# Optimization experiments

Measured on AMD Instinct MI355X. Metric: run time of the kernel, lower is better.

The kernel has to match this reference:

```python
import jax, jax.numpy as jnp
import numpy as np

L, D, H, N, B2 = 9, 256, 4, 1024, 4   # layers, embed dim, heads, keypoints, 2*pairs
HD = D // H
THR = 0.1
MAXM = 50


def _linear(x, W, b):
    return x @ W.T + b


def _ln(x, g, b, eps=1e-5):
    m = jnp.mean(x, -1, keepdims=True)
    v = jnp.var(x, -1, keepdims=True)
    return (x - m) * jax.lax.rsqrt(v + eps) * g + b


def _ffn(x, w1, b1, g, bb, w2, b2):
    h = _linear(x, w1, b1)
    h = jax.nn.gelu(_ln(h, g, bb), approximate=False)
    return _linear(h, w2, b2)


def _mha(q, k, v):
    b, nq, _ = q.shape
    nk = k.shape[1]
    qh = q.reshape(b, nq, H, HD)
    kh = k.reshape(b, nk, H, HD)
    vh = v.reshape(b, nk, H, HD)
    s = jnp.einsum('bqhd,bkhd->bhqk', qh, kh) * (1.0 / np.float32(np.sqrt(HD)))
    a = jax.nn.softmax(s, -1)
    return jnp.einsum('bhqk,bkhd->bqhd', a, vh).reshape(b, nq, D)


def _rotate_half(qk):  # qk: [b, n, D, 2]
    b, n, _, _ = qk.shape
    r = qk.reshape(b, n, H, HD // 2, 2, 2)
    r = jnp.stack([-r[..., 1, :], r[..., 0, :]], axis=4)
    return r.reshape(b, n, D, 2)


def _posenc(kpts, Wr):
    proj = kpts @ Wr.T                    # [b, n, HD//2]
    def expand(t):
        t = jnp.repeat(t, 2, axis=-1)     # interleave -> [b, n, HD]
        return jnp.tile(t, (1, 1, H))     # -> [b, n, D]
    return jnp.stack([expand(jnp.cos(proj)), expand(jnp.sin(proj))])  # [2, b, n, D]


def _forward(kpts, desc, posenc_Wr,
             sWqkv_w, sWqkv_b, sOut_w, sOut_b, sF1_w, sF1_b, sLN_g, sLN_b, sF2_w, sF2_b,
             cQK_w, cQK_b, cV_w, cV_b, cOut_w, cOut_b, cF1_w, cF1_b, cLN_g, cLN_b, cF2_w, cF2_b,
             fp_w, fp_b, match_w, match_b):
    enc = _posenc(kpts, posenc_Wr)
    x = desc
    idx = np.arange(B2)
    swap = idx // 2 * 2 + (1 - idx % 2)   # swap images within each pair
    for i in range(L):
        # ---- self attention with cached rotary encoding ----
        b, n, _ = x.shape
        qkv = _linear(x, sWqkv_w[i], sWqkv_b[i]).reshape(b, n, D, 3)
        qk, v = qkv[..., :2], qkv[..., 2]
        qk = enc[0][..., None] * qk + enc[1][..., None] * _rotate_half(qk)
        ctx = _mha(qk[..., 0], qk[..., 1], v)
        msg = _linear(ctx, sOut_w[i], sOut_b[i])
        x = x + _ffn(jnp.concatenate([x, msg], -1),
                     sF1_w[i], sF1_b[i], sLN_g[i], sLN_b[i], sF2_w[i], sF2_b[i])
        # ---- cross attention between images of each pair ----
        qk = _linear(x, cQK_w[i], cQK_b[i])
        v = _linear(x, cV_w[i], cV_b[i])
        m = _mha(qk, qk[swap], v[swap])
        m = _linear(m, cOut_w[i], cOut_b[i])
        x = x + _ffn(jnp.concatenate([x, m], -1),
                     cF1_w[i], cF1_b[i], cLN_g[i], cLN_b[i], cF2_w[i], cF2_b[i])
    # ---- match assignment: sigmoid log double softmax ----
    md = _linear(x, fp_w, fp_b) / (D ** 0.25)
    sim = jnp.einsum('bnd,bmd->bnm', md[0::2], md[1::2])
    z = _linear(x, match_w, match_b)      # [B2, N, 1]
    cert = jax.nn.log_sigmoid(z[0::2]) + jnp.swapaxes(jax.nn.log_sigmoid(z[1::2]), 1, 2)
    return jax.nn.log_softmax(sim, 2) + jax.nn.log_softmax(sim, 1) + cert


def _filter_matches(scores):
    B = scores.shape[0]
    m0 = jnp.argmax(scores, 2)
    m1 = jnp.argmax(scores, 1)
    mscores = jnp.exp(jnp.max(scores, 2))
    mutual = jnp.arange(N)[None, :] == jnp.take_along_axis(m1, m0, 1)
    masked = mscores * ((mscores > THR) & mutual).astype(mscores.dtype)
    topk_scores, topk_idx = jax.lax.top_k(masked, MAXM)
    topk_m1 = jnp.take_along_axis(m0, topk_idx, 1)
    b_idx = jnp.broadcast_to(jnp.arange(B)[:, None], (B, MAXM))
    matches = jnp.stack([b_idx, topk_idx, topk_m1], 2)
    return matches[0], topk_scores[0]


def setup_inputs() -> dict:
    key = jax.random.key(0)
    ks = iter(jax.random.split(key, 48))
    def w(shape, scale=0.02):
        return jax.random.normal(next(ks), shape, jnp.float32) * scale
    inp = {
        'kpts': jax.random.normal(next(ks), (B2, N, 2), jnp.float32),
        'desc': jax.random.normal(next(ks), (B2, N, D), jnp.float32),
        'posenc_Wr': w((HD // 2, 2), 1.0),  # std = gamma**-2 = 1
        'sWqkv_w': w((L, 3 * D, D)), 'sWqkv_b': w((L, 3 * D)),
        'sOut_w': w((L, D, D)), 'sOut_b': w((L, D)),
        'sF1_w': w((L, 2 * D, 2 * D)), 'sF1_b': w((L, 2 * D)),
        'sLN_g': jnp.ones((L, 2 * D), jnp.float32), 'sLN_b': jnp.zeros((L, 2 * D), jnp.float32),
        'sF2_w': w((L, D, 2 * D)), 'sF2_b': w((L, D)),
        'cQK_w': w((L, D, D)), 'cQK_b': w((L, D)),
        'cV_w': w((L, D, D)), 'cV_b': w((L, D)),
        'cOut_w': w((L, D, D)), 'cOut_b': w((L, D)),
        'cF1_w': w((L, 2 * D, 2 * D)), 'cF1_b': w((L, 2 * D)),
        'cLN_g': jnp.ones((L, 2 * D), jnp.float32), 'cLN_b': jnp.zeros((L, 2 * D), jnp.float32),
        'cF2_w': w((L, D, 2 * D)), 'cF2_b': w((L, D)),
        'fp_w': w((D, D)), 'fp_b': w((D,)),
        'match_w': w((1, D)), 'match_b': w((1,)),
    }
    return inp


def reference(kpts, desc, posenc_Wr,
              sWqkv_w, sWqkv_b, sOut_w, sOut_b, sF1_w, sF1_b, sLN_g, sLN_b, sF2_w, sF2_b,
              cQK_w, cQK_b, cV_w, cV_b, cOut_w, cOut_b, cF1_w, cF1_b, cLN_g, cLN_b, cF2_w, cF2_b,
              fp_w, fp_b, match_w, match_b):
    scores = _forward(kpts, desc, posenc_Wr,
                      sWqkv_w, sWqkv_b, sOut_w, sOut_b, sF1_w, sF1_b, sLN_g, sLN_b, sF2_w, sF2_b,
                      cQK_w, cQK_b, cV_w, cV_b, cOut_w, cOut_b, cF1_w, cF1_b, cLN_g, cLN_b, cF2_w, cF2_b,
                      fp_w, fp_b, match_w, match_b)
    matches, mscores = _filter_matches(scores)
    return scores, matches, mscores
```

## Files before the change

### kernel.cpp

```cpp
#include <hip/hip_runtime.h>
#include <hip/hip_bf16.h>
#include <math.h>

typedef __hip_bfloat16 bf16;
typedef unsigned short ushort;
typedef unsigned int u32;
typedef __attribute__((ext_vector_type(8))) short s8b;
typedef __attribute__((ext_vector_type(4))) short s4b;
typedef __attribute__((ext_vector_type(4))) float f4v;

#define Nc 1024
#define Dc 256
#define MA 4096

__device__ __forceinline__ float tofl(float v){ return v; }
__device__ __forceinline__ float tofl(bf16 v){ return __bfloat162float(v); }

__device__ __forceinline__ ushort rneu(float f){
  unsigned u = __float_as_uint(f);
  unsigned r = (u + 0x7fffu + ((u>>16)&1u)) >> 16;
  return (ushort)r;
}
__device__ __forceinline__ float ubf(ushort h){ return __uint_as_float(((unsigned)h)<<16); }

__device__ __forceinline__ float fexp2(float x){
#if __has_builtin(__builtin_amdgcn_exp2f)
  return __builtin_amdgcn_exp2f(x);
#else
  return exp2f(x);
#endif
}

__global__ void k_detect(const void* p, int* flag){
  if(threadIdx.x==0 && blockIdx.x==0){
    *flag = (((const ushort*)p)[0] == 0x3F80) ? 0 : 1;
  }
}

template<typename TIN>
__device__ void gemm_body(const float* A, const TIN* B, const TIN* bias, float* C,
                          int M, int Nout, int K, int lda, int ldb, int ldc,
                          float alpha, int accum, int dolog){
  __shared__ float As[32][33];
  __shared__ float Bs[32][33];
  int tx = threadIdx.x, ty = threadIdx.y;
  int tid = ty*16 + tx;
  int n0 = blockIdx.x*32, m0 = blockIdx.y*32;
  int lr = tid >> 3;
  int lc = (tid & 7) * 4;
  float acc00=0.f, acc01=0.f, acc10=0.f, acc11=0.f;
  for(int kk=0; kk<K; kk+=32){
    int m = m0 + lr, n = n0 + lr;
#pragma unroll
    for(int j=0;j<4;j++){
      int k = kk + lc + j;
      As[lr][lc+j] = (m < M && k < K) ? A[(size_t)m*lda + k] : 0.f;
      Bs[lr][lc+j] = (n < Nout && k < K) ? tofl(B[(size_t)n*ldb + k]) : 0.f;
    }
    __syncthreads();
#pragma unroll
    for(int k=0;k<32;k++){
      float a0 = As[ty][k],   a1 = As[ty+16][k];
      float b0 = Bs[tx][k],   b1 = Bs[tx+16][k];
      acc00 += a0*b0; acc01 += a0*b1; acc10 += a1*b0; acc11 += a1*b1;
    }
    __syncthreads();
  }
#define STORE(mm,nn,acc) do{ int m_=(mm), n_=(nn); if(m_<M && n_<Nout){ \
    float r = (acc) + (bias ? tofl(bias[n_]) : 0.f); r *= alpha; \
    if(dolog) r = fminf(r,0.f) - log1pf(expf(-fabsf(r))); \
    if(accum) C[(size_t)m_*ldc + n_] += r; else C[(size_t)m_*ldc + n_] = r; } }while(0)
  STORE(m0+ty,    n0+tx,    acc00);
  STORE(m0+ty,    n0+tx+16, acc01);
  STORE(m0+ty+16, n0+tx,    acc10);
  STORE(m0+ty+16, n0+tx+16, acc11);
#undef STORE
}

__global__ __launch_bounds__(256)
void k_gemm_w(const int* flag, const float* A, const void* Bb, long boff,
              const void* biasb, long biasoff, float* C,
              int M, int Nout, int K, int lda, int ldb, int ldc,
              float alpha, int accum, int dolog){
  if(*flag){
    const float* B = ((const float*)Bb) + boff;
    const float* bi = biasb ? ((const float*)biasb) + biasoff : nullptr;
    gemm_body<float>(A, B, bi, C, M, Nout, K, lda, ldb, ldc, alpha, accum, dolog);
  }else{
    const bf16* B = ((const bf16*)Bb) + boff;
    const bf16* bi = biasb ? ((const bf16*)biasb) + biasoff : nullptr;
    gemm_body<bf16>(A, B, bi, C, M, Nout, K, lda, ldb, ldc, alpha, accum, dolog);
  }
}

template<typename TIN>
__device__ void cast2_body(const void* in_, float* x, ushort* xh, ushort* xl, int n){
  const TIN* in = (const TIN*)in_;
  int i = blockIdx.x*256 + threadIdx.x;
  if(i >= n) return;
  float f = tofl(in[i]);
  x[i] = f;
  ushort h = rneu(f);
  xh[i] = h; xl[i] = rneu(f - ubf(h));
}
__global__ void k_cast2(const int* flag, const void* in, float* x, ushort* xh, ushort* xl, int n){
  if(*flag) cast2_body<float>(in, x, xh, xl, n); else cast2_body<bf16>(in, x, xh, xl, n);
}

template<typename TIN>
__device__ void splitw_body(const void* src_, long off, ushort* dh, ushort* dl, int n){
  const TIN* src = ((const TIN*)src_) + off;
  int i = blockIdx.x*256 + threadIdx.x;
  if(i >= n) return;
  float f = tofl(src[i]);
  ushort h = rneu(f);
  dh[i] = h; dl[i] = rneu(f - ubf(h));
}
__global__ void k_splitw(const int* flag, const void* src, long off, ushort* dh, ushort* dl, int n){
  if(*flag) splitw_body<float>(src, off, dh, dl, n); else splitw_body<bf16>(src, off, dh, dl, n);
}
template<typename TIN>
__device__ void biasf_body(const void* src_, long off, float* dst, int n){
  const TIN* src = ((const TIN*)src_) + off;
  int i = blockIdx.x*256 + threadIdx.x;
  if(i < n) dst[i] = tofl(src[i]);
}
__global__ void k_biasf(const int* flag, const void* src, long off, float* dst, int n){
  if(*flag) biasf_body<float>(src, off, dst, n); else biasf_body<bf16>(src, off, dst, n);
}

template<typename TIN>
__device__ void rotcs_body(const void* kpts_, const void* Wr_, float* cs){
  int i = blockIdx.x*256 + threadIdx.x;
  if(i >= MA*32) return;
  int m = i >> 5, p = i & 31;
  const TIN* kpts = (const TIN*)kpts_;
  const TIN* Wr   = (const TIN*)Wr_;
  float kx = tofl(kpts[m*2]), ky = tofl(kpts[m*2+1]);
  float proj = kx*tofl(Wr[p*2]) + ky*tofl(Wr[p*2+1]);
  cs[(size_t)m*64 + p*2    ] = cosf(proj);
  cs[(size_t)m*64 + p*2 + 1] = sinf(proj);
}
__global__ void k_rotcs(const int* flag, const void* kpts, const void* Wr, float* cs){
  if(*flag) rotcs_body<float>(kpts, Wr, cs); else rotcs_body<bf16>(kpts, Wr, cs);
}

template<typename TIN>
__device__ void wsl_body(int L, const void* p0,const void* p1,const void* p2,const void* p3,
                         const void* p4,const void* p5,const void* p6,const void* p7,const void* p8,
                         const void* b0,const void* b1,const void* b2,const void* b3,const void* b4,
                         const void* b5,const void* b6,const void* b7,const void* b8,
                         ushort* WH, ushort* WL, float* WB){
  int idx = blockIdx.x*256 + threadIdx.x;
  if(idx < 311296){
    int i = idx*4;
    const TIN* s = nullptr;
    const TIN* tb = nullptr; int trow = 0, tcol = 0;
    if(i < 196608){
      int nr = i >> 8, col = i & 255;
      int sr = (nr < 256) ? nr*3 : (nr < 512) ? (nr-256)*3+1 : (nr-512)*3+2;
      s = (const TIN*)p0 + (size_t)L*196608 + sr*256 + col;
    }
    else if(i < 262144){ int li = i-196608; tb = (const TIN*)p1 + (size_t)L*65536; trow = li>>8; tcol = li&255; }
    else if(i < 524288)  s = (const TIN*)p2 + (size_t)L*262144 + (i-262144);
    else if(i < 655360)  s = (const TIN*)p3 + (size_t)L*131072 + (i-524288);
    else if(i < 720896)  s = (const TIN*)p4 + (size_t)L*65536  + (i-655360);
    else if(i < 786432)  s = (const TIN*)p5 + (size_t)L*65536  + (i-720896);
    else if(i < 851968){ int li = i-786432; tb = (const TIN*)p6 + (size_t)L*65536; trow = li>>8; tcol = li&255; }
    else if(i < 1114112) s = (const TIN*)p7 + (size_t)L*262144 + (i-851968);
    else                 s = (const TIN*)p8 + (size_t)L*131072 + (i-1114112);
    float f[4];
    if(tb){
#pragma unroll
      for(int j=0;j<4;j++) f[j] = tofl(tb[(size_t)(tcol+j)*256 + trow]);
    } else if constexpr(sizeof(TIN) == 4){
      f4v v = *(const f4v*)s;
      f[0]=v[0]; f[1]=v[1]; f[2]=v[2]; f[3]=v[3];
    } else {
      s4b v = *(const s4b*)s;
#pragma unroll
      for(int j=0;j<4;j++) f[j] = __uint_as_float(((u32)(ushort)v[j])<<16);
    }
    s4b hv, lv;
#pragma unroll
    for(int j=0;j<4;j++){
      ushort h = rneu(f[j]);
      hv[j] = (short)h;
      lv[j] = (short)rneu(f[j] - ubf(h));
    }
    *(s4b*)&WH[i] = hv;
    *(s4b*)&WL[i] = lv;
  } else if(idx < 311296 + 3328){
    int j = idx - 311296;
    const TIN* s;
    if(j < 768){
      int sj = (j < 256) ? j*3 : (j < 512) ? (j-256)*3+1 : (j-512)*3+2;
      s = (const TIN*)b0 + (size_t)L*768 + sj;
    }
    else if(j < 1024)  s = (const TIN*)b1 + (size_t)L*256 + (j-768);
    else if(j < 1536)  s = (const TIN*)b2 + (size_t)L*512 + (j-1024);
    else if(j < 1792)  s = (const TIN*)b3 + (size_t)L*256 + (j-1536);
    else if(j < 2048)  s = (const TIN*)b4 + (size_t)L*256 + (j-1792);
    else if(j < 2304)  s = (const TIN*)b5 + (size_t)L*256 + (j-2048);
    else if(j < 2560)  s = (const TIN*)b6 + (size_t)L*256 + (j-2304);
    else if(j < 3072)  s = (const TIN*)b7 + (size_t)L*512 + (j-2560);
    else               s = (const TIN*)b8 + (size_t)L*256 + (j-3072);
    WB[j] = tofl(*s);
  }
}
__global__ void k_wsplit(const int* flag, int L0, long strW, long strB,
    const void* p0,const void* p1,const void* p2,const void* p3,const void* p4,
    const void* p5,const void* p6,const void* p7,const void* p8,
    const void* b0,const void* b1,const void* b2,const void* b3,const void* b4,
    const void* b5,const void* b6,const void* b7,const void* b8,
    ushort* WH, ushort* WL, float* WB){
  int L = L0 + blockIdx.y;
  ushort* WHl = WH + (size_t)blockIdx.y*strW;
  ushort* WLl = WL + (size_t)blockIdx.y*strW;
  float*  WBl = WB + (size_t)blockIdx.y*strB;
  if(*flag) wsl_body<float>(L,p0,p1,p2,p3,p4,p5,p6,p7,p8,b0,b1,b2,b3,b4,b5,b6,b7,b8,WHl,WLl,WBl);
  else      wsl_body<bf16>(L,p0,p1,p2,p3,p4,p5,p6,p7,p8,b0,b1,b2,b3,b4,b5,b6,b7,b8,WHl,WLl,WBl);
}

__global__ __launch_bounds__(256)
void k_bcomb(const ushort* __restrict__ WH, const ushort* __restrict__ WL,
             float* WB, long strW, long strB){
  __shared__ float bo[256];
  int bx = blockIdx.x;
  int c = blockIdx.y;
  int L = c >> 1, br = c & 1;
  size_t wbase = (size_t)L*strW + (br ? 851968 : 262144);
  float* WBl = WB + (size_t)L*strB;
  float* b1 = WBl + (br ? 2560 : 1024);
  const float* bout = WBl + (br ? 2304 : 768);
  int t = threadIdx.x;
  bo[t] = bout[t];
  __syncthreads();
  int o = bx*64 + (t>>2);
  int p = t & 3;
  size_t rb = wbase + (size_t)o*512 + 256;
  float s = 0.f;
  for(int j=p*64; j<p*64+64; j++){
    s += (ubf(WH[rb+j]) + ubf(WL[rb+j])) * bo[j];
  }
  s += __shfl_xor(s,1);
  s += __shfl_xor(s,2);
  if(p==0) b1[o] += s;
}

template<int MT>
__global__ __launch_bounds__(256)
void k_gemm_mxT(const ushort* __restrict__ Ah, const ushort* __restrict__ Al,
                const ushort* __restrict__ A2h, const ushort* __restrict__ A2l, int lda,
                const ushort* __restrict__ Bh, const ushort* __restrict__ Bl, int ldb,
                const float* __restrict__ bias, float alpha,
                float* C, int ldc, int accum,
                ushort* Ch, ushort* Cl, int lds,
                ushort* keh, ushort* kel, const float* __restrict__ cs,
                ushort* vth, ushort* vtl,
                int K, int mode){
  constexpr int MFR = MT/16;
  constexpr int NACC = MFR*2;
  constexpr int MFH = MFR/2;
  __shared__ __align__(16) ushort LB[(2*MT+128)*72];
  int t = threadIdx.x;
  int n0 = blockIdx.x*64, m0 = blockIdx.y*MT;
  size_t wofs4 = 0;
  if(mode == 4){
    int by = blockIdx.y;
    int combo = by >> 4;
    m0 = (by & 15) * MT;
    int Lc = combo >> 1, br = combo & 1;
    size_t basec = (size_t)Lc * (size_t)lds;
    wofs4 = basec + (br ? 851968 : 262144) + 256;
    size_t oofs = basec + (br ? 786432 : 196608);
    Bh = Ah + oofs; Bl = Al + oofs; ldb = 256;
    Ah = Ah + wofs4; Al = Al + wofs4; lda = 512;
  }
  int w = t>>6, lane = t&63, quad = lane>>4, l15 = lane&15;
  int kg = w>>1, nh = w&1;
  int brow = t>>2, bc16 = (t&3)*16;
  int arow = (MT==64) ? (t>>2) : (t>>3);
  int acol = (MT==64) ? ((t&3)*16) : ((t&7)*8);
  f4v acc[NACC];
  f4v zz = {0.f,0.f,0.f,0.f};
#pragma unroll
  for(int j=0;j<NACC;j++) acc[j] = zz;
  int rounds = K >> 6;

  s8b r0,r1,r2,r3,r4,r5,r6,r7;
  auto gload = [&](int r){
    int k0 = r*64;
    const ushort* ah = Ah; const ushort* al = Al; int kloc = k0;
    if(A2h && k0 >= 256){ ah = A2h; al = A2l; kloc = k0 - 256; }
    const ushort* aph = &ah[(size_t)(m0+arow)*lda + kloc + acol];
    const ushort* apl = &al[(size_t)(m0+arow)*lda + kloc + acol];
    const ushort* bph = &Bh[(size_t)(n0+brow)*ldb + k0 + bc16];
    const ushort* bpl = &Bl[(size_t)(n0+brow)*ldb + k0 + bc16];
    r0 = *(const s8b*)aph;
    r2 = *(const s8b*)apl;
    if(MT==64){ r1 = *(const s8b*)(aph+8); r3 = *(const s8b*)(apl+8); }
    r4 = *(const s8b*)bph;   r5 = *(const s8b*)(bph+8);
    r6 = *(const s8b*)bpl;   r7 = *(const s8b*)(bpl+8);
  };
  auto writeS = [&](){
    *(s8b*)&LB[(arow)*72 + acol]        = r0;
    *(s8b*)&LB[(MT+arow)*72 + acol]     = r2;
    if(MT==64){
      *(s8b*)&LB[(arow)*72 + acol+8]    = r1;
      *(s8b*)&LB[(MT+arow)*72 + acol+8] = r3;
    }
    *(s8b*)&LB[(2*MT+brow)*72 + bc16]      = r4;
    *(s8b*)&LB[(2*MT+brow)*72 + bc16+8]    = r5;
    *(s8b*)&LB[(2*MT+64+brow)*72 + bc16]   = r6;
    *(s8b*)&LB[(2*MT+64+brow)*72 + bc16+8] = r7;
  };

  gload(0);
  for(int r=0; r<rounds; r++){
    __syncthreads();
    writeS();
    __syncthreads();
    s8b afh[MFR], afl[MFR], bfh[2], bfl[2];
#pragma unroll
    for(int mf=0;mf<MFR;mf++){
      afh[mf] = *(s8b*)&LB[(mf*16+l15)*72 + kg*32+quad*8];
      afl[mf] = *(s8b*)&LB[(MT+mf*16+l15)*72 + kg*32+quad*8];
    }
#pragma unroll
    for(int nf=0;nf<2;nf++){
      bfh[nf] = *(s8b*)&LB[(2*MT+nh*32+nf*16+l15)*72 + kg*32+quad*8];
      bfl[nf] = *(s8b*)&LB[(2*MT+64+nh*32+nf*16+l15)*72 + kg*32+quad*8];
    }
    if(r+1 < rounds) gload(r+1);
#pragma unroll
    for(int mf=0;mf<MFR;mf++){
#pragma unroll
      for(int nf=0;nf<2;nf++){
        int a = mf*2+nf;
        acc[a] = __builtin_amdgcn_mfma_f32_16x16x32_bf16(afh[mf], bfh[nf], acc[a], 0,0,0);
        acc[a] = __builtin_amdgcn_mfma_f32_16x16x32_bf16(afh[mf], bfl[nf], acc[a], 0,0,0);
        acc[a] = __builtin_amdgcn_mfma_f32_16x16x32_bf16(afl[mf], bfh[nf], acc[a], 0,0,0);
      }
    }
  }
  __syncthreads();
  f4v* scr = (f4v*)LB;
#pragma unroll
  for(int f=0;f<NACC;f++) scr[(w*NACC+f)*64 + lane] = acc[f];
  __syncthreads();
  int pw = w^2;
#pragma unroll
  for(int f=0;f<NACC;f++){
    f4v o = scr[(pw*NACC+f)*64 + lane];
    acc[f] += o;
  }

  bool vblk = (mode == 1 && n0 >= 512) || (mode == 3 && n0 >= 256);
  if(vblk){
    __syncthreads();
    u32* tp = (u32*)LB;
#pragma unroll
    for(int mi=0;mi<MFH;mi++){
      int mf = kg*MFH + mi;
#pragma unroll
      for(int nf=0;nf<2;nf++){
        f4v a = acc[mf*2+nf];
#pragma unroll
        for(int rr=0;rr<4;rr++){
          int ml = mf*16 + quad*4 + rr;
          int nl = nh*32 + nf*16 + l15;
          float val = a[rr];
          if(bias) val += bias[n0 + nl];
          val *= alpha;
          ushort hh = rneu(val);
          ushort ll = rneu(val - ubf(hh));
          tp[nl*(MT+1) + ml] = (u32)hh | ((u32)ll << 16);
        }
      }
    }
    __syncthreads();
    int b = m0 >> 10;
    int mloc = m0 & 1023;
    int d0 = n0 - ((mode == 1) ? 512 : 256);
    constexpr int NPASS = (MT==64) ? 2 : 1;
#pragma unroll
    for(int pass=0; pass<NPASS; pass++){
      int row, col;
      if(MT==64){ row = (t>>3) + pass*32; col = (t&7)*8; }
      else      { row = t>>2;             col = (t&3)*8; }
      int d = d0 + row;
      u32 c0=tp[row*(MT+1)+col+0], c1=tp[row*(MT+1)+col+1], c2=tp[row*(MT+1)+col+2], c3=tp[row*(MT+1)+col+3];
      u32 c4=tp[row*(MT+1)+col+4], c5=tp[row*(MT+1)+col+5], c6=tp[row*(MT+1)+col+6], c7=tp[row*(MT+1)+col+7];
      s8b hi, lo;
      hi[0]=(short)(c0&0xffff); lo[0]=(short)(c0>>16);
      hi[1]=(short)(c1&0xffff); lo[1]=(short)(c1>>16);
      hi[2]=(short)(c2&0xffff); lo[2]=(short)(c2>>16);
      hi[3]=(short)(c3&0xffff); lo[3]=(short)(c3>>16);
      hi[4]=(short)(c4&0xffff); lo[4]=(short)(c4>>16);
      hi[5]=(short)(c5&0xffff); lo[5]=(short)(c5>>16);
      hi[6]=(short)(c6&0xffff); lo[6]=(short)(c6>>16);
      hi[7]=(short)(c7&0xffff); lo[7]=(short)(c7>>16);
      size_t go = ((size_t)((b*4 + (d>>6))*64 + (d&63)))*1024 + mloc + col;
      *(s8b*)&vth[go] = hi;
      *(s8b*)&vtl[go] = lo;
    }
    return;
  }

#pragma unroll
  for(int mi=0;mi<MFH;mi++){
    int mf = kg*MFH + mi;
#pragma unroll
    for(int nf=0;nf<2;nf++){
      f4v a = acc[mf*2+nf];
#pragma unroll
      for(int rr=0;rr<4;rr++){
        int m = m0 + mf*16 + quad*4 + rr;
        int n = n0 + nh*32 + nf*16 + l15;
        float val = a[rr];
        if(bias) val += bias[n];
        val *= alpha;
        if(mode == 1){
          int d = (n < 256) ? n : (n - 256);
          const float* csp = cs + (size_t)m*64 + (d & 62);
          float cc = csp[0], ssn = csp[1];
          float pv = __shfl_xor(val, 1);
          float rv = (d & 1) ? (cc*val + ssn*pv) : (cc*val - ssn*pv);
          ushort hh = rneu(rv);
          ushort* dh = (n < 256) ? Ch : keh;
          ushort* dl = (n < 256) ? Cl : kel;
          size_t gi = (size_t)m*256 + d;
          dh[gi] = hh; dl[gi] = rneu(rv - ubf(hh));
        } else if(mode == 3){
          ushort hh = rneu(val);
          Ch[(size_t)m*256 + n] = hh;
          Cl[(size_t)m*256 + n] = rneu(val - ubf(hh));
        } else if(mode == 4){
          ushort hh = rneu(val);
          size_t gi = wofs4 + (size_t)m*512 + n;
          Ch[gi] = hh;
          Cl[gi] = rneu(val - ubf(hh));
        } else {
          if(C){
            size_t ci = (size_t)m*ldc + n;
            if(accum) val += C[ci];
            C[ci] = val;
          }
          if(Ch){
            ushort hh = rneu(val);
            Ch[(size_t)m*lds + n] = hh;
            Cl[(size_t)m*lds + n] = rneu(val - ubf(hh));
          }
        }
      }
    }
  }
}

#define FSC 0.18033688011112042f
__global__ __launch_bounds__(256)
void k_flashmx(const ushort* __restrict__ qh_, const ushort* __restrict__ ql_,
               const ushort* __restrict__ kh_, const ushort* __restrict__ kl_,
               const ushort* __restrict__ vth_, const ushort* __restrict__ vtl_,
               ushort* __restrict__ cth, ushort* __restrict__ ctl, int bxor,
               float* __restrict__ PO, float* __restrict__ PML, int nch){
  int qt = blockIdx.x, z = blockIdx.y, ch = blockIdx.z;
  int b = z>>2, h = z&3;
  int bk = b ^ bxor;
  __shared__ __align__(16) ushort Kh[64][72], Kl[64][72], Vh[64][72], Vl[64][72];
  int t = threadIdx.x, w = t>>6, lane = t&63, quad = lane>>4, l15 = lane&15;
  ushort* Psw = &Kh[w*16][0];
  s8b qfh[2], qfl[2];
  {
    size_t row = (size_t)b*1024 + qt*64 + w*16 + l15;
    const ushort* qrh = qh_ + row*256 + h*64;
    const ushort* qrl = ql_ + row*256 + h*64;
    qfh[0] = *(const s8b*)(qrh + quad*8);
    qfh[1] = *(const s8b*)(qrh + 32 + quad*8);
    qfl[0] = *(const s8b*)(qrl + quad*8);
    qfl[1] = *(const s8b*)(qrl + 32 + quad*8);
  }
  float m_i[4] = {-1e30f,-1e30f,-1e30f,-1e30f};
  float l_i[4] = {0.f,0.f,0.f,0.f};
  f4v O[4];
  f4v zz = {0.f,0.f,0.f,0.f};
#pragma unroll
  for(int dt=0;dt<4;dt++) O[dt] = zz;

  s8b rK0,rK1,rK2,rK3, rV0,rV1,rV2,rV3;
  auto stage_load = [&](int kt){
#pragma unroll
    for(int i=0;i<4;i++){
      int c = t + i*256;
      int half = c>>9, row = (c>>3)&63, o8 = (c&7)*8;
      const s8b* src = (const s8b*)((half ? kl_ : kh_) +
                       ((size_t)(bk*1024 + kt*64 + row))*256 + h*64 + o8);
      if(i==0) rK0=*src; else if(i==1) rK1=*src; else if(i==2) rK2=*src; else rK3=*src;
    }
#pragma unroll
    for(int i=0;i<4;i++){
      int c = t + i*256;
      int half = c>>9, d = (c>>3)&63, o8 = (c&7)*8;
      const s8b* src = (const s8b*)((half ? vtl_ : vth_) +
                       ((size_t)((bk*4+h)*64 + d))*1024 + kt*64 + o8);
      if(i==0) rV0=*src; else if(i==1) rV1=*src; else if(i==2) rV2=*src; else rV3=*src;
    }
  };
  auto stage_write = [&](){
#pragma unroll
    for(int i=0;i<4;i++){
      int c = t + i*256;
      int half = c>>9, row = (c>>3)&63, o8 = (c&7)*8;
      s8b v = (i==0)?rK0:(i==1)?rK1:(i==2)?rK2:rK3;
      if(half) *(s8b*)&Kl[row][o8] = v;
      else     *(s8b*)&Kh[row][o8] = v;
    }
#pragma unroll
    for(int i=0;i<4;i++){
      int c = t + i*256;
      int half = c>>9, d = (c>>3)&63, o8 = (c&7)*8;
      s8b v = (i==0)?rV0:(i==1)?rV1:(i==2)?rV2:rV3;
      if(half) *(s8b*)&Vl[d][o8] = v;
      else     *(s8b*)&Vh[d][o8] = v;
    }
  };

  int ktn = 16/nch;
  int kt0 = ch*ktn;
  stage_load(kt0);
  for(int kt=kt0; kt<kt0+ktn; kt++){
    __syncthreads();
    stage_write();
    __syncthreads();
    if(kt+1 < kt0+ktn) stage_load(kt+1);
    f4v s[4];
#pragma unroll
    for(int nt=0;nt<4;nt++) s[nt] = zz;
#pragma unroll
    for(int nt=0;nt<4;nt++){
#pragma unroll
      for(int k2=0;k2<2;k2++){
        s8b fbh = *(s8b*)&Kh[nt*16+l15][k2*32 + quad*8];
        s8b fbl = *(s8b*)&Kl[nt*16+l15][k2*32 + quad*8];
        s[nt] = __builtin_amdgcn_mfma_f32_16x16x32_bf16(qfh[k2], fbh, s[nt], 0,0,0);
        s[nt] = __builtin_amdgcn_mfma_f32_16x16x32_bf16(qfh[k2], fbl, s[nt], 0,0,0);
        s[nt] = __builtin_amdgcn_mfma_f32_16x16x32_bf16(qfl[k2], fbh, s[nt], 0,0,0);
      }
    }
    __syncthreads();
#pragma unroll
    for(int rr=0;rr<4;rr++){
      float v0=s[0][rr]*FSC, v1=s[1][rr]*FSC, v2=s[2][rr]*FSC, v3=s[3][rr]*FSC;
      float mx = fmaxf(fmaxf(v0,v1), fmaxf(v2,v3));
      mx = fmaxf(mx, __shfl_xor(mx,1));
      mx = fmaxf(mx, __shfl_xor(mx,2));
      mx = fmaxf(mx, __shfl_xor(mx,4));
      mx = fmaxf(mx, __shfl_xor(mx,8));
      float mnew = fmaxf(m_i[rr], mx);
      float al = fexp2(m_i[rr] - mnew);
      float p0 = fexp2(v0-mnew), p1 = fexp2(v1-mnew), p2 = fexp2(v2-mnew), p3 = fexp2(v3-mnew);
      float ls = p0+p1+p2+p3;
      ls += __shfl_xor(ls,1);
      ls += __shfl_xor(ls,2);
      ls += __shfl_xor(ls,4);
      ls += __shfl_xor(ls,8);
      l_i[rr] = l_i[rr]*al + ls;
      m_i[rr] = mnew;
#pragma unroll
      for(int dt=0;dt<4;dt++) O[dt][rr] *= al;
      int prow = quad*4 + rr;
      Psw[prow*72 +  0 + l15] = rneu(p0);
      Psw[prow*72 + 16 + l15] = rneu(p1);
      Psw[prow*72 + 32 + l15] = rneu(p2);
      Psw[prow*72 + 48 + l15] = rneu(p3);
    }
    s8b pf0 = *(s8b*)&Psw[l15*72 + quad*8];
    s8b pf1 = *(s8b*)&Psw[l15*72 + 32 + quad*8];
#pragma unroll
    for(int dt=0;dt<4;dt++){
#pragma unroll
      for(int k2=0;k2<2;k2++){
        s8b fvh = *(s8b*)&Vh[dt*16+l15][k2*32 + quad*8];
        s8b fvl = *(s8b*)&Vl[dt*16+l15][k2*32 + quad*8];
        s8b pf = k2 ? pf1 : pf0;
        O[dt] = __builtin_amdgcn_mfma_f32_16x16x32_bf16(pf, fvh, O[dt], 0,0,0);
        O[dt] = __builtin_amdgcn_mfma_f32_16x16x32_bf16(pf, fvl, O[dt], 0,0,0);
      }
    }
  }
  if(nch == 1){
#pragma unroll
    for(int rr=0;rr<4;rr++){
      float inv = 1.f / l_i[rr];
      int row = qt*64 + w*16 + quad*4 + rr;
#pragma unroll
      for(int dt=0;dt<4;dt++){
        float val = O[dt][rr]*inv;
        size_t gi = ((size_t)b*1024 + row)*256 + h*64 + dt*16 + l15;
        ushort hh = rneu(val);
        cth[gi] = hh; ctl[gi] = rneu(val - ubf(hh));
      }
    }
  } else {
    size_t tb = (size_t)(z*16+qt)*nch + ch;
    float* po  = PO  + tb*4096;
    float* pml = PML + tb*128;
#pragma unroll
    for(int rr=0;rr<4;rr++){
      int row = w*16 + quad*4 + rr;
#pragma unroll
      for(int dt=0;dt<4;dt++){
        po[row*64 + dt*16 + l15] = O[dt][rr];
      }
      if(l15 == 0){
        pml[row]      = m_i[rr];
        pml[64 + row] = l_i[rr];
      }
    }
  }
}

__global__ __launch_bounds__(256)
void k_fmerge(const float* __restrict__ PO, const float* __restrict__ PML,
              ushort* __restrict__ cth, ushort* __restrict__ ctl){
  int qt = blockIdx.x, z = blockIdx.y;
  int b = z>>2, h = z&3;
  int t = threadIdx.x;
  int row = t>>2, dg = (t&3)*16;
  size_t tb0 = (size_t)(z*16+qt)*4;
  float m0 = PML[(tb0+0)*128 + row], m1 = PML[(tb0+1)*128 + row];
  float m2 = PML[(tb0+2)*128 + row], m3 = PML[(tb0+3)*128 + row];
  float M = fmaxf(fmaxf(m0,m1), fmaxf(m2,m3));
  float w0 = fexp2(m0-M), w1 = fexp2(m1-M), w2 = fexp2(m2-M), w3 = fexp2(m3-M);
  float L = PML[(tb0+0)*128 + 64 + row]*w0 + PML[(tb0+1)*128 + 64 + row]*w1
          + PML[(tb0+2)*128 + 64 + row]*w2 + PML[(tb0+3)*128 + 64 + row]*w3;
  float inv = 1.f/L;
  const f4v* p0 = (const f4v*)(PO + (tb0+0)*4096 + row*64 + dg);
  const f4v* p1 = (const f4v*)(PO + (tb0+1)*4096 + row*64 + dg);
  const f4v* p2 = (const f4v*)(PO + (tb0+2)*4096 + row*64 + dg);
  const f4v* p3 = (const f4v*)(PO + (tb0+3)*4096 + row*64 + dg);
  size_t gi = ((size_t)b*1024 + qt*64 + row)*256 + h*64 + dg;
#pragma unroll
  for(int j=0;j<4;j++){
    f4v o = p0[j]*w0 + p1[j]*w1 + p2[j]*w2 + p3[j]*w3;
#pragma unroll
    for(int e=0;e<4;e++){
      float val = o[e]*inv;
      ushort hh = rneu(val);
      cth[gi + j*4 + e] = hh;
      ctl[gi + j*4 + e] = rneu(val - ubf(hh));
    }
  }
}

template<typename TIN>
__device__ void ln2_body(const float* h, ushort* hh, ushort* hl, const TIN* g, const TIN* bb){
  __shared__ float ws8[8];
  int r = blockIdx.x; int t = threadIdx.x;
  int w = t>>6, lane = t&63;
  const float* row = h + (size_t)r*512;
  float a = row[t], b_ = row[t+256];
  float s = a + b_;
#pragma unroll
  for(int off=1; off<64; off<<=1) s += __shfl_xor(s, off);
  if(lane==0) ws8[w] = s;
  __syncthreads();
  float mean = (ws8[0]+ws8[1]+ws8[2]+ws8[3])*(1.f/512.f);
  float da = a-mean, db = b_-mean;
  float v = da*da + db*db;
#pragma unroll
  for(int off=1; off<64; off<<=1) v += __shfl_xor(v, off);
  if(lane==0) ws8[4+w] = v;
  __syncthreads();
  float rstd = rsqrtf((ws8[4]+ws8[5]+ws8[6]+ws8[7])*(1.f/512.f) + 1e-5f);
  float na = da*rstd*tofl(g[t])     + tofl(bb[t]);
  float nb = db*rstd*tofl(g[t+256]) + tofl(bb[t+256]);
  float ga = 0.5f*na*(1.f + erff(na*0.70710678f));
  float gb = 0.5f*nb*(1.f + erff(nb*0.70710678f));
  size_t base = (size_t)r*512;
  ushort u0 = rneu(ga); hh[base+t] = u0; hl[base+t] = rneu(ga - ubf(u0));
  ushort u1 = rneu(gb); hh[base+t+256] = u1; hl[base+t+256] = rneu(gb - ubf(u1));
}
__global__ void k_ln_gelu2(const int* flag, const float* h, ushort* hh, ushort* hl,
                           const void* gb, long goff, const void* bbb, long boff){
  if(*flag) ln2_body<float>(h, hh, hl, ((const float*)gb)+goff, ((const float*)bbb)+boff);
  else      ln2_body<bf16>(h, hh, hl, ((const bf16*)gb)+goff, ((const bf16*)bbb)+boff);
}

__global__ void k_lse_cols2(const float* __restrict__ simbase, float* __restrict__ clseb){
  __shared__ float Rm[16][16], Rs[16][16];
  int blk = blockIdx.x;
  int p = blk >> 6, bx = blk & 63;
  const float* sim = simbase + (size_t)p*1048576;
  float* clse = clseb + p*1024;
  int t = threadIdx.x;
  int c = t & 15, s = t >> 4;
  int col = bx*16 + c;
  const float* base = sim + col;
  float mx = -1e30f, sum = 0.f;
  for(int n=s*64; n<s*64+64; n++){
    float v = base[(size_t)n*1024];
    if(v > mx){ sum = sum*expf(mx - v) + 1.f; mx = v; }
    else sum += expf(v - mx);
  }
  Rm[s][c] = mx; Rs[s][c] = sum; __syncthreads();
  for(int off=8; off>0; off>>=1){
    if(s < off){
      float m2 = Rm[s+off][c], s2 = Rs[s+off][c];
      float m1 = Rm[s][c], s1 = Rs[s][c];
      float m = fmaxf(m1, m2);
      Rm[s][c] = m;
      Rs[s][c] = s1*expf(m1-m) + s2*expf(m2-m);
    }
    __syncthreads();
  }
  if(s == 0) clse[col] = Rm[0][c] + logf(Rs[0][c]);
}

__global__ __launch_bounds__(256)
void k_final2r(float* __restrict__ out,
               const float* __restrict__ clse, const float* __restrict__ lsg,
               int* __restrict__ m0, float* __restrict__ msc){
  __shared__ float ws4[4];
  __shared__ float bsum[4];
  int blk = blockIdx.x;
  int p = blk >> 10, n = blk & 1023;
  int t = threadIdx.x;
  int w = t>>6, lane = t&63;
  size_t base = (size_t)blk*1024;
  float v0 = out[base+t], v1 = out[base+t+256], v2 = out[base+t+512], v3 = out[base+t+768];
  float mx = fmaxf(fmaxf(v0,v1),fmaxf(v2,v3));
#pragma unroll
  for(int off=1; off<64; off<<=1) mx = fmaxf(mx, __shfl_xor(mx, off));
  if(lane==0) ws4[w] = mx;
  __syncthreads();
  float bm = fmaxf(fmaxf(ws4[0],ws4[1]),fmaxf(ws4[2],ws4[3]));
  float s = expf(v0-bm)+expf(v1-bm)+expf(v2-bm)+expf(v3-bm);
#pragma unroll
  for(int off=1; off<64; off<<=1) s += __shfl_xor(s, off);
  if(lane==0) bsum[w] = s;
  __syncthreads();
  float rl = bm + logf(bsum[0]+bsum[1]+bsum[2]+bsum[3]);
  float lgn = lsg[p*2048 + n];
  const float* lgm = lsg + p*2048 + 1024;
  const float* cl = clse + p*1024;
  float bv = -1e30f; int bi = 0;
  float nv;
  int m;
  m = t;     nv = 2.f*v0 - rl - cl[m] + lgn + lgm[m]; out[base+m] = nv; if(nv > bv){ bv = nv; bi = m; }
  m = t+256; nv = 2.f*v1 - rl - cl[m] + lgn + lgm[m]; out[base+m] = nv; if(nv > bv){ bv = nv; bi = m; }
  m = t+512; nv = 2.f*v2 - rl - cl[m] + lgn + lgm[m]; out[base+m] = nv; if(nv > bv){ bv = nv; bi = m; }
  m = t+768; nv = 2.f*v3 - rl - cl[m] + lgn + lgm[m]; out[base+m] = nv; if(nv > bv){ bv = nv; bi = m; }
  if(p) return;
#pragma unroll
  for(int off=1; off<64; off<<=1){
    float v2_ = __shfl_xor(bv, off); int i2 = __shfl_xor(bi, off);
    if(v2_ > bv || (v2_ == bv && i2 < bi)){ bv = v2_; bi = i2; }
  }
  __shared__ float wv[4]; __shared__ int wi[4];
  if(lane==0){ wv[w]=bv; wi[w]=bi; }
  __syncthreads();
  if(t==0){
#pragma unroll
    for(int k=1;k<4;k++){
      if(wv[k] > wv[0] || (wv[k]==wv[0] && wi[k] < wi[0])){ wv[0]=wv[k]; wi[0]=wi[k]; }
    }
    m0[n] = wi[0]; msc[n] = expf(wv[0]);
  }
}

__global__ void k_amax_cols2(const float* __restrict__ sc, int* __restrict__ m1){
  __shared__ float Rv[16][16]; __shared__ int Ri[16][16];
  int t = threadIdx.x;
  int c = t & 15, s = t >> 4;
  int col = blockIdx.x*16 + c;
  float bv = -1e30f; int bi = 0;
  for(int n=s*64; n<s*64+64; n++){
    float v = sc[(size_t)n*1024 + col];
    if(v > bv){ bv = v; bi = n; }
  }
  Rv[s][c]=bv; Ri[s][c]=bi; __syncthreads();
  for(int off=8; off>0; off>>=1){
    if(s < off){
      if(Rv[s+off][c] > Rv[s][c]){ Rv[s][c]=Rv[s+off][c]; Ri[s][c]=Ri[s+off][c]; }
    }
    __syncthreads();
  }
  if(s == 0) m1[col] = Ri[0][c];
}

__global__ __launch_bounds__(128)
void k_topk(const int* __restrict__ m0, const int* __restrict__ m1,
            const float* __restrict__ msc, float* __restrict__ out){
  __shared__ float V[1024];
  int t = threadIdx.x;
  for(int i2=t; i2<1024; i2+=128){
    float mv = msc[i2];
    V[i2] = (mv > 0.1f && m1[m0[i2]] == i2) ? mv : 0.f;
  }
  __syncthreads();
  int i = blockIdx.x*128 + t;
  float vi = V[i];
  int r = 0;
#pragma unroll 8
  for(int j=0;j<1024;j++){
    float vj = V[j];
    r += (vj > vi || (vj == vi && j < i)) ? 1 : 0;
  }
  if(r < 50){
    out[2*Nc*Nc + r*3 + 0] = 0.f;
    out[2*Nc*Nc + r*3 + 1] = (float)i;
    out[2*Nc*Nc + r*3 + 2] = (float)m0[i];
    out[2*Nc*Nc + 150 + r] = vi;
  }
}

extern "C" void kernel_launch(void* const* d_in, const int* in_sizes, int n_in,
                              void* d_out, int out_size, void* d_ws, size_t ws_size,
                              hipStream_t stream){
  const void* kpts    = d_in[0];
  const void* desc    = d_in[1];
  const void* Wr      = d_in[2];
  const void* sWqkv_w = d_in[3];
  const void* sWqkv_b = d_in[4];
  const void* sOut_w  = d_in[5];
  const void* sOut_b  = d_in[6];
  const void* sF1_w   = d_in[7];
  const void* sF1_b   = d_in[8];
  const void* sLN_g   = d_in[9];
  const void* sLN_b   = d_in[10];
  const void* sF2_w   = d_in[11];
  const void* sF2_b   = d_in[12];
  const void* cQK_w   = d_in[13];
  const void* cQK_b   = d_in[14];
  const void* cV_w    = d_in[15];
  const void* cV_b    = d_in[16];
  const void* cOut_w  = d_in[17];
  const void* cOut_b  = d_in[18];
  const void* cF1_w   = d_in[19];
  const void* cF1_b   = d_in[20];
  const void* cLN_g   = d_in[21];
  const void* cLN_b   = d_in[22];
  const void* cF2_w   = d_in[23];
  const void* cF2_b   = d_in[24];
  const void* fp_w    = d_in[25];
  const void* fp_b    = d_in[26];
  const void* match_w = d_in[27];
  const void* match_b = d_in[28];

  float* ws  = (float*)d_ws;
  float* out = (float*)d_out;
  int* flag = (int*)d_ws;
  float* zbuf = ws + 64;
  float* clse = ws + 6208;
  float* msc  = ws + 12352;
  int*   m0i  = (int*)(ws + 13376);
  int*   m1i  = (int*)(ws + 14400);

  bool presplit = ws_size >= (size_t)20759552*4 + 1024;
  size_t wW = presplit ? 5603328 : 622592;
  size_t wB = presplit ? 32768   : 4096;

  size_t o = 16384;
  ushort* WH = (ushort*)(ws + o); o += wW;
  ushort* WL = (ushort*)(ws + o); o += wW;
  float*  WB = ws + o;            o += wB;
  ushort* fpWH = (ushort*)(ws + o); o += 32768;
  ushort* fpWL = (ushort*)(ws + o); o += 32768;
  float*  fpB  = ws + o;            o += 1024;
  float*  x  = ws + o;              o += 1048576;
  ushort* xh = (ushort*)(ws + o);   o += 524288;
  ushort* xl = (ushort*)(ws + o);   o += 524288;
  float*  hbuf = ws + o;            o += 2097152;
  ushort* qsh = (ushort*)(ws + o);  o += 524288;
  ushort* qsl = (ushort*)(ws + o);  o += 524288;
  ushort* ksh = (ushort*)(ws + o);  o += 524288;
  ushort* ksl = (ushort*)(ws + o);  o += 524288;
  ushort* vth = (ushort*)(ws + o);  o += 524288;
  ushort* vtl = (ushort*)(ws + o);  o += 524288;
  ushort* cth = (ushort*)(ws + o);  o += 524288;
  ushort* ctl = (ushort*)(ws + o);  o += 524288;
  ushort* mgh = (ushort*)(ws + o);  o += 524288;
  ushort* mgl = (ushort*)(ws + o);  o += 524288;
  ushort* hsh = qsh;
  ushort* hsl = ksh;
  ushort* mdh = cth;
  ushort* mdl = ctl;
  (void)mgh; (void)mgl;

  float* cs = out;

  float* PO  = ws + o;
  float* PML = ws + o + 4194304;
  int nch = (ws_size >= (size_t)(20759552 + 4194304 + 131072)*4 + 1024) ? 4 : 1;

  auto MX = [&](const ushort* Ah, const ushort* Al, const ushort* A2h, const ushort* A2l,
                int lda, const ushort* Bh, const ushort* Bl, int ldb,
                const float* bias, float alpha, float* C, int ldc, int accum,
                ushort* Ch, ushort* Cl, int lds,
                ushort* keh, ushort* kel, ushort* vh, ushort* vl,
                int M, int Nout, int K, int mode, int mt){
    dim3 g(Nout/64, M/mt);
    if(mt == 32)
      k_gemm_mxT<32><<<g, 256, 0, stream>>>(Ah,Al,A2h,A2l,lda,Bh,Bl,ldb,bias,alpha,C,ldc,accum,
                                            Ch,Cl,lds,keh,kel,cs,vh,vl,K,mode);
    else
      k_gemm_mxT<64><<<g, 256, 0, stream>>>(Ah,Al,A2h,A2l,lda,Bh,Bl,ldb,bias,alpha,C,ldc,accum,
                                            Ch,Cl,lds,keh,kel,cs,vh,vl,K,mode);
  };
  auto FLASH = [&](const ushort* qh, const ushort* ql, const ushort* kh, const ushort* kl,
                   int bxor){
    k_flashmx<<<dim3(16,16,nch), 256, 0, stream>>>(qh,ql,kh,kl,vth,vtl, cth,ctl, bxor,
                                                   PO, PML, nch);
    if(nch == 4) k_fmerge<<<dim3(16,16), 256, 0, stream>>>(PO, PML, cth, ctl);
  };
  auto FOLD = [&](int ncombo, long strW){
    k_bcomb<<<dim3(8, ncombo), 256, 0, stream>>>(WH, WL, WB, strW, presplit ? 3328 : 0);
    k_gemm_mxT<32><<<dim3(4, ncombo*16), 256, 0, stream>>>(
        WH, WL, nullptr, nullptr, 0, nullptr, nullptr, 0,
        nullptr, 1.f, nullptr, 0, 0,
        WH, WL, (int)strW, nullptr, nullptr, cs, nullptr, nullptr, 256, 4);
  };

  k_detect<<<1, 64, 0, stream>>>(sLN_g, flag);
  k_splitw<<<(65536+255)/256, 256, 0, stream>>>(flag, fp_w, 0, fpWH, fpWL, 65536);
  k_biasf<<<1, 256, 0, stream>>>(flag, fp_b, 0, fpB, 256);
  k_cast2<<<(MA*Dc+255)/256, 256, 0, stream>>>(flag, desc, x, xh, xl, MA*Dc);
  k_rotcs<<<(MA*32+255)/256, 256, 0, stream>>>(flag, kpts, Wr, cs);

  if(presplit){
    dim3 g((311296+3328+255)/256, 9);
    k_wsplit<<<g, 256, 0, stream>>>(flag, 0, 1245184, 3328,
      sWqkv_w, sOut_w, sF1_w, sF2_w, cQK_w, cV_w, cOut_w, cF1_w, cF2_w,
      sWqkv_b, sOut_b, sF1_b, sF2_b, cQK_b, cV_b, cOut_b, cF1_b, cF2_b,
      WH, WL, WB);
    FOLD(18, 1245184);
  }

  for(int i=0;i<9;i++){
    if(!presplit){
      dim3 g((311296+3328+255)/256, 1);
      k_wsplit<<<g, 256, 0, stream>>>(flag, i, 0, 0,
        sWqkv_w, sOut_w, sF1_w, sF2_w, cQK_w, cV_w, cOut_w, cF1_w, cF2_w,
        sWqkv_b, sOut_b, sF1_b, sF2_b, cQK_b, cV_b, cOut_b, cF1_b, cF2_b,
        WH, WL, WB);
      FOLD(2, 0);
    }
    const ushort* WHl = presplit ? WH + (size_t)i*1245184 : WH;
    const ushort* WLl = presplit ? WL + (size_t)i*1245184 : WL;
    const float*  WBl = presplit ? WB + (size_t)i*3328    : WB;

    MX(xh,xl,nullptr,nullptr,256, WHl+0,WLl+0,256, WBl+0, 1.f,
       nullptr,0,0, qsh,qsl,0, ksh,ksl, vth,vtl, MA,768,256, 1, 32);
    FLASH(qsh,qsl,ksh,ksl, 0);
    MX(xh,xl,cth,ctl,256, WHl+262144,WLl+262144,512, WBl+1024, 1.f,
       hbuf,512,0, nullptr,nullptr,0, nullptr,nullptr, nullptr,nullptr, MA,512,512, 0, 32);
    k_ln_gelu2<<<MA, 256, 0, stream>>>(flag, hbuf, hsh, hsl, sLN_g, (long)i*512, sLN_b, (long)i*512);
    MX(hsh,hsl,nullptr,nullptr,512, WHl+524288,WLl+524288,512, WBl+1536, 1.f,
       x,256,1, xh,xl,256, nullptr,nullptr, nullptr,nullptr, MA,256,512, 0, 32);
    MX(xh,xl,nullptr,nullptr,256, WHl+655360,WLl+655360,256, WBl+1792, 1.f,
       nullptr,0,0, qsh,qsl,0, nullptr,nullptr, vth,vtl, MA,512,256, 3, 32);
    FLASH(qsh,qsl,qsh,qsl, 1);
    MX(xh,xl,cth,ctl,256, WHl+851968,WLl+851968,512, WBl+2560, 1.f,
       hbuf,512,0, nullptr,nullptr,0, nullptr,nullptr, nullptr,nullptr, MA,512,512, 0, 32);
    k_ln_gelu2<<<MA, 256, 0, stream>>>(flag, hbuf, hsh, hsl, cLN_g, (long)i*512, cLN_b, (long)i*512);
    MX(hsh,hsl,nullptr,nullptr,512, WHl+1114112,WLl+1114112,512, WBl+3072, 1.f,
       x,256,1, xh,xl,256, nullptr,nullptr, nullptr,nullptr, MA,256,512, 0, 32);
  }

  MX(xh,xl,nullptr,nullptr,256, fpWH,fpWL,256, fpB, 0.25f,
     nullptr,0,0, mdh,mdl,256, nullptr,nullptr, nullptr,nullptr, MA,256,256, 0, 32);
  k_gemm_w<<<dim3(1,128), dim3(16,16), 0, stream>>>(flag, x, match_w, 0, match_b, 0,
                                                    zbuf, MA, 1, 256, 256, 256, 1, 1.f, 0, 1);
  MX(mdh,mdl,nullptr,nullptr,256, mdh + (size_t)1024*256, mdl + (size_t)1024*256, 256,
     nullptr, 1.f, out,1024,0, nullptr,nullptr,0, nullptr,nullptr, nullptr,nullptr, 1024,1024,256, 0, 32);
  MX(mdh + (size_t)2048*256, mdl + (size_t)2048*256,nullptr,nullptr,256,
     mdh + (size_t)3072*256, mdl + (size_t)3072*256, 256,
     nullptr, 1.f, out+1048576,1024,0, nullptr,nullptr,0, nullptr,nullptr, nullptr,nullptr, 1024,1024,256, 0, 32);

  k_lse_cols2<<<128, 256, 0, stream>>>(out, clse);
  k_final2r<<<2048, 256, 0, stream>>>(out, clse, zbuf, m0i, msc);
  k_amax_cols2<<<64, 256, 0, stream>>>(out, m1i);
  k_topk<<<8, 128, 0, stream>>>(m0i, m1i, msc, out);
}
```

Baseline: 1.831 ms.

## Fuse LayerNorm+GELU into the second FFN GEMM's A-operand load

Removes the standalone LayerNorm+GELU kernel and its bf16 hi/lo split round-trip. The second FFN GEMM now computes per-row mean and rstd in a prologue, then normalizes, applies GELU and splits on the fly while loading A tiles. LN gamma/beta are pre-converted to float once. The trade-off is that each of the 4 column blocks redoes the row statistics and erf work (4x redundant), and the A load becomes fp32 reads plus ALU work on the GEMM critical path. Variance is now computed as E[x^2]-mean^2, which is less numerically stable.

```diff
diff --git a/kernel.cpp b/kernel.cpp
--- a/kernel.cpp
+++ b/kernel.cpp
@@ -263,6 +263,7 @@
   constexpr int NACC = MFR*2;
   constexpr int MFH = MFR/2;
   __shared__ __align__(16) ushort LB[(2*MT+128)*72];
+  __shared__ float mstat[32][2];
   int t = threadIdx.x;
   int n0 = blockIdx.x*64, m0 = blockIdx.y*MT;
   size_t wofs4 = 0;
@@ -288,18 +289,55 @@
   for(int j=0;j<NACC;j++) acc[j] = zz;
   int rounds = K >> 6;
 
+  if(MT==32 && mode==5){
+    int pr = t>>3, pc0 = (t&7)*64;
+    const float* hr = cs + (size_t)(m0+pr)*512 + pc0;
+    float sum=0.f, sq=0.f;
+    for(int j=0;j<64;j+=4){
+      f4v v = *(const f4v*)&hr[j];
+      sum += v[0]+v[1]+v[2]+v[3];
+      sq  += v[0]*v[0]+v[1]*v[1]+v[2]*v[2]+v[3]*v[3];
+    }
+    sum += __shfl_xor(sum,1); sum += __shfl_xor(sum,2); sum += __shfl_xor(sum,4);
+    sq  += __shfl_xor(sq,1);  sq  += __shfl_xor(sq,2);  sq  += __shfl_xor(sq,4);
+    if((t&7)==0){
+      float mean = sum*(1.f/512.f);
+      mstat[pr][0] = mean;
+      mstat[pr][1] = rsqrtf(sq*(1.f/512.f) - mean*mean + 1e-5f);
+    }
+    __syncthreads();
+  }
+
   s8b r0,r1,r2,r3,r4,r5,r6,r7;
   auto gload = [&](int r){
     int k0 = r*64;
-    const ushort* ah = Ah; const ushort* al = Al; int kloc = k0;
-    if(A2h && k0 >= 256){ ah = A2h; al = A2l; kloc = k0 - 256; }
-    const ushort* aph = &ah[(size_t)(m0+arow)*lda + kloc + acol];
-    const ushort* apl = &al[(size_t)(m0+arow)*lda + kloc + acol];
+    if(MT==32 && mode==5){
+      const float* hr = cs + (size_t)(m0+arow)*512 + k0 + acol;
+      f4v a0 = *(const f4v*)hr;
+      f4v a1 = *(const f4v*)(hr+4);
+      const float* gg  = ((const float*)keh) + k0 + acol;
+      const float* bb2 = ((const float*)kel) + k0 + acol;
+      float mean = mstat[arow][0], rstd = mstat[arow][1];
+      float av[8] = {a0[0],a0[1],a0[2],a0[3],a1[0],a1[1],a1[2],a1[3]};
+#pragma unroll
+      for(int j=0;j<8;j++){
+        float na = (av[j]-mean)*rstd*gg[j] + bb2[j];
+        float ga = 0.5f*na*(1.f + erff(na*0.70710678f));
+        ushort h = rneu(ga);
+        r0[j] = (short)h;
+        r2[j] = (short)rneu(ga - ubf(h));
+      }
+    } else {
+      const ushort* ah = Ah; const ushort* al = Al; int kloc = k0;
+      if(A2h && k0 >= 256){ ah = A2h; al = A2l; kloc = k0 - 256; }
+      const ushort* aph = &ah[(size_t)(m0+arow)*lda + kloc + acol];
+      const ushort* apl = &al[(size_t)(m0+arow)*lda + kloc + acol];
+      r0 = *(const s8b*)aph;
+      r2 = *(const s8b*)apl;
+      if(MT==64){ r1 = *(const s8b*)(aph+8); r3 = *(const s8b*)(apl+8); }
+    }
     const ushort* bph = &Bh[(size_t)(n0+brow)*ldb + k0 + bc16];
     const ushort* bpl = &Bl[(size_t)(n0+brow)*ldb + k0 + bc16];
-    r0 = *(const s8b*)aph;
-    r2 = *(const s8b*)apl;
-    if(MT==64){ r1 = *(const s8b*)(aph+8); r3 = *(const s8b*)(apl+8); }
     r4 = *(const s8b*)bph;   r5 = *(const s8b*)(bph+8);
     r6 = *(const s8b*)bpl;   r7 = *(const s8b*)(bpl+8);
   };
@@ -654,40 +692,6 @@
   }
 }
 
-template<typename TIN>
-__device__ void ln2_body(const float* h, ushort* hh, ushort* hl, const TIN* g, const TIN* bb){
-  __shared__ float ws8[8];
-  int r = blockIdx.x; int t = threadIdx.x;
-  int w = t>>6, lane = t&63;
-  const float* row = h + (size_t)r*512;
-  float a = row[t], b_ = row[t+256];
-  float s = a + b_;
-#pragma unroll
-  for(int off=1; off<64; off<<=1) s += __shfl_xor(s, off);
-  if(lane==0) ws8[w] = s;
-  __syncthreads();
-  float mean = (ws8[0]+ws8[1]+ws8[2]+ws8[3])*(1.f/512.f);
-  float da = a-mean, db = b_-mean;
-  float v = da*da + db*db;
-#pragma unroll
-  for(int off=1; off<64; off<<=1) v += __shfl_xor(v, off);
-  if(lane==0) ws8[4+w] = v;
-  __syncthreads();
-  float rstd = rsqrtf((ws8[4]+ws8[5]+ws8[6]+ws8[7])*(1.f/512.f) + 1e-5f);
-  float na = da*rstd*tofl(g[t])     + tofl(bb[t]);
-  float nb = db*rstd*tofl(g[t+256]) + tofl(bb[t+256]);
-  float ga = 0.5f*na*(1.f + erff(na*0.70710678f));
-  float gb = 0.5f*nb*(1.f + erff(nb*0.70710678f));
-  size_t base = (size_t)r*512;
-  ushort u0 = rneu(ga); hh[base+t] = u0; hl[base+t] = rneu(ga - ubf(u0));
-  ushort u1 = rneu(gb); hh[base+t+256] = u1; hl[base+t+256] = rneu(gb - ubf(u1));
-}
-__global__ void k_ln_gelu2(const int* flag, const float* h, ushort* hh, ushort* hl,
-                           const void* gb, long goff, const void* bbb, long boff){
-  if(*flag) ln2_body<float>(h, hh, hl, ((const float*)gb)+goff, ((const float*)bbb)+boff);
-  else      ln2_body<bf16>(h, hh, hl, ((const bf16*)gb)+goff, ((const bf16*)bbb)+boff);
-}
-
 __global__ void k_lse_cols2(const float* __restrict__ simbase, float* __restrict__ clseb){
   __shared__ float Rm[16][16], Rs[16][16];
   int blk = blockIdx.x;
@@ -883,11 +887,12 @@
   ushort* ctl = (ushort*)(ws + o);  o += 524288;
   ushort* mgh = (ushort*)(ws + o);  o += 524288;
   ushort* mgl = (ushort*)(ws + o);  o += 524288;
-  ushort* hsh = qsh;
-  ushort* hsl = ksh;
   ushort* mdh = cth;
   ushort* mdl = ctl;
-  (void)mgh; (void)mgl;
+  (void)mgl;
+
+  float* lngA = (float*)mgh;
+  float* lnbA = lngA + 9216;
 
   float* cs = out;
 
@@ -922,10 +927,23 @@
         nullptr, 1.f, nullptr, 0, 0,
         WH, WL, (int)strW, nullptr, nullptr, cs, nullptr, nullptr, 256, 4);
   };
+  auto FFN2 = [&](const ushort* Bh, const ushort* Bl, const float* bias,
+                  const float* lng, const float* lnb){
+    k_gemm_mxT<32><<<dim3(4, 128), 256, 0, stream>>>(
+        nullptr, nullptr, nullptr, nullptr, 0,
+        Bh, Bl, 512,
+        bias, 1.f, x, 256, 1,
+        xh, xl, 256,
+        (ushort*)lng, (ushort*)lnb, hbuf, nullptr, nullptr, 512, 5);
+  };
 
   k_detect<<<1, 64, 0, stream>>>(sLN_g, flag);
   k_splitw<<<(65536+255)/256, 256, 0, stream>>>(flag, fp_w, 0, fpWH, fpWL, 65536);
   k_biasf<<<1, 256, 0, stream>>>(flag, fp_b, 0, fpB, 256);
+  k_biasf<<<18, 256, 0, stream>>>(flag, sLN_g, 0, lngA, 4608);
+  k_biasf<<<18, 256, 0, stream>>>(flag, cLN_g, 0, lngA + 4608, 4608);
+  k_biasf<<<18, 256, 0, stream>>>(flag, sLN_b, 0, lnbA, 4608);
+  k_biasf<<<18, 256, 0, stream>>>(flag, cLN_b, 0, lnbA + 4608, 4608);
   k_cast2<<<(MA*Dc+255)/256, 256, 0, stream>>>(flag, desc, x, xh, xl, MA*Dc);
   k_rotcs<<<(MA*32+255)/256, 256, 0, stream>>>(flag, kpts, Wr, cs);
 
@@ -956,17 +974,13 @@
     FLASH(qsh,qsl,ksh,ksl, 0);
     MX(xh,xl,cth,ctl,256, WHl+262144,WLl+262144,512, WBl+1024, 1.f,
        hbuf,512,0, nullptr,nullptr,0, nullptr,nullptr, nullptr,nullptr, MA,512,512, 0, 32);
-    k_ln_gelu2<<<MA, 256, 0, stream>>>(flag, hbuf, hsh, hsl, sLN_g, (long)i*512, sLN_b, (long)i*512);
-    MX(hsh,hsl,nullptr,nullptr,512, WHl+524288,WLl+524288,512, WBl+1536, 1.f,
-       x,256,1, xh,xl,256, nullptr,nullptr, nullptr,nullptr, MA,256,512, 0, 32);
+    FFN2(WHl+524288, WLl+524288, WBl+1536, lngA + i*512, lnbA + i*512);
     MX(xh,xl,nullptr,nullptr,256, WHl+655360,WLl+655360,256, WBl+1792, 1.f,
        nullptr,0,0, qsh,qsl,0, nullptr,nullptr, vth,vtl, MA,512,256, 3, 32);
     FLASH(qsh,qsl,qsh,qsl, 1);
     MX(xh,xl,cth,ctl,256, WHl+851968,WLl+851968,512, WBl+2560, 1.f,
        hbuf,512,0, nullptr,nullptr,0, nullptr,nullptr, nullptr,nullptr, MA,512,512, 0, 32);
-    k_ln_gelu2<<<MA, 256, 0, stream>>>(flag, hbuf, hsh, hsl, cLN_g, (long)i*512, cLN_b, (long)i*512);
-    MX(hsh,hsl,nullptr,nullptr,512, WHl+1114112,WLl+1114112,512, WBl+3072, 1.f,
-       x,256,1, xh,xl,256, nullptr,nullptr, nullptr,nullptr, MA,256,512, 0, 32);
+    FFN2(WHl+1114112, WLl+1114112, WBl+3072, lngA + 4608 + i*512, lnbA + 4608 + i*512);
   }
 
   MX(xh,xl,nullptr,nullptr,256, fpWH,fpWL,256, fpB, 0.25f,
```

Measured after the change: 2.240 ms. 22.4% more time.
